# Kernel tuning notes

Measured on AMD Instinct MI355X. Metric: run time of the kernel, lower is better.

The kernel has to match this reference:

```python
import jax, jax.numpy as jnp
import numpy as np

N_NODES = 20000
N_EDGES = 200000
D_MODEL = 128
N_HEADS = 8
N_LAYERS = 2  # num_gnn - 1 concat layers


def setup_inputs() -> dict:
    key = jax.random.key(0)
    ks = jax.random.split(key, 12)
    s = 0.05  # keep activations well-scaled across residual layers
    hd = D_MODEL // N_HEADS  # 16
    return {
        "x": jax.random.normal(ks[0], (N_NODES, D_MODEL), jnp.float32),
        "src": jax.random.randint(ks[1], (N_EDGES,), 0, N_NODES),
        "dst": jax.random.randint(ks[2], (N_EDGES,), 0, N_NODES),
        "Ws": jax.random.normal(ks[3], (N_LAYERS, D_MODEL, D_MODEL), jnp.float32) * s,
        "als": jax.random.normal(ks[4], (N_LAYERS, N_HEADS, hd), jnp.float32) * s,
        "ars": jax.random.normal(ks[5], (N_LAYERS, N_HEADS, hd), jnp.float32) * s,
        "bs": jax.random.normal(ks[6], (N_LAYERS, D_MODEL), jnp.float32) * s,
        "W_last": jax.random.normal(ks[7], (D_MODEL, N_HEADS * D_MODEL), jnp.float32) * s,
        "al_last": jax.random.normal(ks[8], (N_HEADS, D_MODEL), jnp.float32) * s,
        "ar_last": jax.random.normal(ks[9], (N_HEADS, D_MODEL), jnp.float32) * s,
        "b_last": jax.random.normal(ks[10], (N_HEADS * D_MODEL,), jnp.float32) * s,
    }


def gat_conv(h, src, dst, W, al, ar, b, num_nodes):
    """DGL GATConv (eval mode, dropout off): returns (N, H, D) head outputs."""
    H, D = al.shape
    feat = (h @ W).reshape(num_nodes, H, D)          # (N,H,D)
    el = jnp.sum(feat * al[None], axis=-1)           # (N,H) attn on src side
    er = jnp.sum(feat * ar[None], axis=-1)           # (N,H) attn on dst side
    e = jax.nn.leaky_relu(el[src] + er[dst], 0.2)    # (E,H)
    # edge softmax over incoming edges of each dst node, per head
    m = jax.ops.segment_max(e, dst, num_segments=num_nodes)  # (N,H)
    p = jnp.exp(e - m[dst])                          # (E,H)
    z = jax.ops.segment_sum(p, dst, num_segments=num_nodes)  # (N,H)
    a = p / z[dst]                                   # (E,H)
    msg = feat[src] * a[..., None]                   # (E,H,D) weighted messages
    rst = jax.ops.segment_sum(msg, dst, num_segments=num_nodes)  # (N,H,D)
    return rst + b.reshape(1, H, D)


def reference(x, src, dst, Ws, als, ars, bs, W_last, al_last, ar_last, b_last):
    N = x.shape[0]
    h = x
    for i in range(N_LAYERS):
        temp = gat_conv(h, src, dst, Ws[i], als[i], ars[i], bs[i], N)  # (N,H,hd)
        h = h + jax.nn.elu(temp.reshape(N, -1))       # concat heads, ELU, residual
    temp = gat_conv(h, src, dst, W_last, al_last, ar_last, b_last, N)  # (N,H,D)
    h = h + jnp.mean(temp, axis=1)                    # mean over heads, residual
    return h
```

## Files before the change

### kernel.cpp

```cpp
#include <hip/hip_runtime.h>
#include <math.h>

#define N_NODES 20000
#define N_EDGES 200000
#define DM 128
#define NH 8

typedef __attribute__((ext_vector_type(8))) short bf16x8;
typedef __attribute__((ext_vector_type(4))) float f32x4;

__device__ __forceinline__ unsigned short f2b(float f) {
  unsigned int u = __float_as_uint(f);
  unsigned int r = (u + 0x7FFFu + ((u >> 16) & 1u)) >> 16;
  return (unsigned short)r;
}
__device__ __forceinline__ float b2f(unsigned short s) {
  return __uint_as_float(((unsigned int)s) << 16);
}

__global__ __launch_bounds__(256) void degzero(int* __restrict__ deg) {
  int i = blockIdx.x * 256 + threadIdx.x;
  if (i < N_NODES) deg[i] = 0;
}

__global__ __launch_bounds__(256) void prep_all(
    const float* __restrict__ x, float* __restrict__ h, unsigned short* __restrict__ hb,
    const int* __restrict__ dstE, int* __restrict__ deg, int* __restrict__ rank,
    const float* __restrict__ Ws, unsigned short* __restrict__ wsz,
    const float* __restrict__ W_last, unsigned short* __restrict__ wpsz,
    const float* __restrict__ al_last, const float* __restrict__ ar_last,
    const float* __restrict__ b_last, unsigned short* __restrict__ wlrsz,
    float* __restrict__ mb) {
  int i = blockIdx.x * 256 + threadIdx.x;
  if (i < (N_NODES * DM) / 4) {
    float4 v = ((const float4*)x)[i];
    ((float4*)h)[i] = v;
    ((ushort4*)hb)[i] = make_ushort4(f2b(v.x), f2b(v.y), f2b(v.z), f2b(v.w));
  }
  if (i < N_EDGES) rank[i] = atomicAdd(&deg[dstE[i]], 1);
  if (i < 2 * 16384) {
    int layer = i >> 14;
    int r = i & 16383;
    int j = r & 7, l = (r >> 3) & 63, f = (r >> 9) & 7, ks = r >> 12;
    int k = ks * 32 + ((l >> 4) << 3) + j;
    int n = f * 16 + (l & 15);
    wsz[i] = f2b(Ws[(size_t)layer * 16384 + k * 128 + n]);
  }
  if (i < 131072) {
    int j = i & 7, l = (i >> 3) & 63, f = (i >> 9) & 7, ks = i >> 12;
    int k = ks * 32 + ((l >> 4) << 3) + j;
    int n = f * 16 + (l & 15);
    int h_ = k >> 7, ko = k & 127;
    wpsz[i] = f2b(W_last[(size_t)ko * 1024 + h_ * 128 + n] * 0.125f);
  }
  if (i < 2048) {
    int j = i & 7, l = (i >> 3) & 63, ks = i >> 9;
    int k = ks * 32 + ((l >> 4) << 3) + j;
    int n = l & 15;
    int hh = n & 7;
    const float* av = (n < 8) ? (al_last + hh * 128) : (ar_last + hh * 128);
    float s = 0.f;
    for (int d = 0; d < 128; ++d) s += W_last[(size_t)k * 1024 + hh * 128 + d] * av[d];
    wlrsz[i] = f2b(s);
  }
  if (i < 128) {
    float s = 0.f;
#pragma unroll
    for (int hh = 0; hh < 8; ++hh) s += b_last[hh * 128 + i];
    mb[i] = s * 0.125f;
  }
}

template <int K>
__device__ __forceinline__ void dev_gemm(int tile, const unsigned short* __restrict__ A,
                                         const unsigned short* __restrict__ Bsz,
                                         unsigned short* __restrict__ Cb,
                                         const float* __restrict__ al,
                                         const float* __restrict__ ar,
                                         float* __restrict__ elr, int lane, int wid) {
  const int wrow = wid & 1, wc = wid >> 1;
  const int r0 = tile * 32;
  const int arow = r0 + wrow * 16 + (lane & 15);
  const int kg = lane >> 4;

  f32x4 acc[4];
#pragma unroll
  for (int fi = 0; fi < 4; ++fi) acc[fi] = {0.f, 0.f, 0.f, 0.f};

  const bf16x8* Ap = (const bf16x8*)(A + (size_t)arow * K + kg * 8);
#pragma unroll 4
  for (int ks = 0; ks < K / 32; ++ks) {
    bf16x8 a = Ap[ks * 4];
#pragma unroll
    for (int fi = 0; fi < 4; ++fi) {
      int f = wc * 4 + fi;
      bf16x8 b = *(const bf16x8*)(Bsz + (((size_t)(ks * 8 + f) * 64 + lane) << 3));
      acc[fi] = __builtin_amdgcn_mfma_f32_16x16x32_bf16(a, b, acc[fi], 0, 0, 0);
    }
  }

  const int rbase = r0 + wrow * 16 + (lane >> 4) * 4;
#pragma unroll
  for (int fi = 0; fi < 4; ++fi) {
    int col = wc * 64 + fi * 16 + (lane & 15);
#pragma unroll
    for (int r = 0; r < 4; ++r) {
      Cb[(size_t)(rbase + r) * DM + col] = f2b(acc[fi][r]);
    }
  }

#pragma unroll
  for (int fi = 0; fi < 4; ++fi) {
    int hh = wc * 4 + fi;
    float alv = al[hh * 16 + (lane & 15)];
    float arv = ar[hh * 16 + (lane & 15)];
#pragma unroll
    for (int r = 0; r < 4; ++r) {
      float pl = acc[fi][r] * alv;
      float pr = acc[fi][r] * arv;
#pragma unroll
      for (int msk = 1; msk < 16; msk <<= 1) {
        pl += __shfl_xor(pl, msk, 64);
        pr += __shfl_xor(pr, msk, 64);
      }
      if ((lane & 15) == 0) {
        int row = rbase + r;
        elr[row * 16 + hh] = pl;
        elr[row * 16 + 8 + hh] = pr;
      }
    }
  }
}

__global__ __launch_bounds__(256) void gemm0_scan(
    const unsigned short* __restrict__ A, const unsigned short* __restrict__ Bsz,
    unsigned short* __restrict__ Cb, const float* __restrict__ al,
    const float* __restrict__ ar, float* __restrict__ elr, const int* __restrict__ deg,
    int* __restrict__ off, int* __restrict__ bbase_g, int* __restrict__ bcur_g) {
  const int bid = blockIdx.x;
  const int GB = N_NODES / 32;
  if (bid < GB) {
    dev_gemm<DM>(bid, A, Bsz, Cb, al, ar, elr, threadIdx.x & 63, threadIdx.x >> 6);
    return;
  }
  __shared__ int part[256];
  __shared__ int hist[4][64];
  const int tid = threadIdx.x;
  const int wv = tid >> 6, lane = tid & 63;
  const int CHUNK = (N_NODES + 255) / 256;
  const int b0 = tid * CHUNK;
  const int b1 = min(N_NODES, b0 + CHUNK);
  if (tid < 64) {
    hist[0][tid] = 0; hist[1][tid] = 0; hist[2][tid] = 0; hist[3][tid] = 0;
  }
  __syncthreads();
  int s = 0;
  for (int idx = b0; idx < b1; ++idx) {
    int d = deg[idx];
    s += d;
    atomicAdd(&hist[wv][min(d, 63)], 1);
  }
  part[tid] = s;
  __syncthreads();
  for (int ofs = 1; ofs < 256; ofs <<= 1) {
    int v = (tid >= ofs) ? part[tid - ofs] : 0;
    __syncthreads();
    part[tid] += v;
    __syncthreads();
  }
  int run = (tid > 0) ? part[tid - 1] : 0;
  for (int idx = b0; idx < b1; ++idx) {
    off[idx] = run;
    run += deg[idx];
  }
  if (tid == 255) off[N_NODES] = part[255];
  if (wv == 0) {
    int c = hist[0][lane] + hist[1][lane] + hist[2][lane] + hist[3][lane];
    int inc = c;
#pragma unroll
    for (int ofs = 1; ofs < 64; ofs <<= 1) {
      int v = __shfl_up(inc, ofs, 64);
      if (lane >= ofs) inc += v;
    }
    bbase_g[lane] = inc - c;
    bcur_g[lane] = 0;
  }
}

__global__ __launch_bounds__(256) void scatter_both(
    const int* __restrict__ srcE, const int* __restrict__ dstE,
    const int* __restrict__ rank, const int* __restrict__ off, int* __restrict__ csr_src,
    const int* __restrict__ deg, const int* __restrict__ bbase_g,
    int* __restrict__ bcur_g, int* __restrict__ perm) {
  __shared__ int lcnt[64];
  __shared__ int gbase[64];
  const int bid = blockIdx.x;
  const int EB = (N_EDGES + 255) / 256;
  if (bid < EB) {
    int e = bid * 256 + threadIdx.x;
    if (e < N_EDGES) csr_src[off[dstE[e]] + rank[e]] = srcE[e];
  } else {
    const int tid = threadIdx.x;
    int idx = (bid - EB) * 256 + tid;
    if (tid < 64) lcnt[tid] = 0;
    __syncthreads();
    int d = 0, lrank = 0;
    bool valid = idx < N_NODES;
    if (valid) {
      d = min(deg[idx], 63);
      lrank = atomicAdd(&lcnt[d], 1);
    }
    __syncthreads();
    if (tid < 64 && lcnt[tid] > 0) gbase[tid] = atomicAdd(&bcur_g[tid], lcnt[tid]);
    __syncthreads();
    if (valid) perm[bbase_g[d] + gbase[d] + lrank] = idx;
  }
}

template <int MODE>
__global__ __launch_bounds__(256) void fused_small(
    const int* __restrict__ perm, const int* __restrict__ off,
    const int* __restrict__ csr_src, const unsigned short* __restrict__ feat,
    const float* __restrict__ elr, const float* __restrict__ bias, float* __restrict__ h,
    unsigned short* __restrict__ hb, const unsigned short* __restrict__ wsz1,
    const float* __restrict__ al1, const float* __restrict__ ar1,
    unsigned short* __restrict__ feat_out, float* __restrict__ elr_out,
    const unsigned short* __restrict__ wlrsz, float* __restrict__ elr2_out) {
  __shared__ float a_lds[4][64];
  __shared__ int s_lds[4][8];
  __shared__ float zi_lds[4][8];
  __shared__ __align__(16) unsigned short nh_lds[4][128];
  __shared__ int pnode[4];
  const int wid = threadIdx.x >> 6;
  const int t = perm[blockIdx.x * 4 + wid];
  const int lane = threadIdx.x & 63;
  const int e_loc = lane >> 3, hh = lane & 7;
  const int hg = lane >> 3;
  const int beg = off[t], end = off[t + 1];
  const float ert = elr[t * 16 + 8 + hh];
  if (lane == 0) pnode[wid] = t;

  int e = beg + e_loc;
  bool val = e < end;
  int s = val ? csr_src[e] : 0;
  float xl = val ? elr[s * 16 + hh] : 0.f;

  float z = 0.f, acc0 = 0.f, acc1 = 0.f;
  for (int base = beg; base < end; base += 8) {
    float ex = 0.f;
    if (val) {
      float xv = xl + ert;
      xv = xv > 0.f ? xv : 0.2f * xv;
      ex = __expf(xv);
    }
    a_lds[wid][lane] = ex;
    if (hh == 0) s_lds[wid][e_loc] = s;
    __builtin_amdgcn_wave_barrier();
    asm volatile("s_waitcnt lgkmcnt(0)" ::: "memory");
    z += ex;
    int en = base + 8 + e_loc;
    bool valn = en < end;
    int sn = valn ? csr_src[en] : 0;
    float xln = valn ? elr[sn * 16 + hh] : 0.f;
    int n = min(8, end - base);
    if (n == 8) {
#pragma unroll
      for (int e2 = 0; e2 < 8; ++e2) {
        int s2 = s_lds[wid][e2];
        float a = a_lds[wid][e2 * 8 + hg];
        unsigned int hv = *(const unsigned int*)&feat[(size_t)s2 * 128 + 2 * lane];
        acc0 += a * b2f((unsigned short)(hv & 0xffffu));
        acc1 += a * b2f((unsigned short)(hv >> 16));
      }
    } else {
      for (int e2 = 0; e2 < n; ++e2) {
        int s2 = s_lds[wid][e2];
        float a = a_lds[wid][e2 * 8 + hg];
        unsigned int hv = *(const unsigned int*)&feat[(size_t)s2 * 128 + 2 * lane];
        acc0 += a * b2f((unsigned short)(hv & 0xffffu));
        acc1 += a * b2f((unsigned short)(hv >> 16));
      }
    }
    __builtin_amdgcn_wave_barrier();
    s = sn;
    xl = xln;
    val = valn;
  }
  z += __shfl_xor(z, 8, 64);
  z += __shfl_xor(z, 16, 64);
  z += __shfl_xor(z, 32, 64);
  if (e_loc == 0) zi_lds[wid][hh] = (z > 0.f) ? 1.f / z : 0.f;
  __builtin_amdgcn_wave_barrier();
  asm volatile("s_waitcnt lgkmcnt(0)" ::: "memory");
  float zi = zi_lds[wid][hg];

  float2 bv = *(const float2*)&bias[2 * lane];
  float v0 = acc0 * zi + bv.x;
  float v1 = acc1 * zi + bv.y;
  v0 = v0 > 0.f ? v0 : expm1f(v0);
  v1 = v1 > 0.f ? v1 : expm1f(v1);
  size_t idx = (size_t)t * 128 + 2 * lane;
  float2 hv = *(const float2*)&h[idx];
  float nh0 = hv.x + v0;
  float nh1 = hv.y + v1;
  *(float2*)&h[idx] = make_float2(nh0, nh1);
  unsigned short b0 = f2b(nh0), b1 = f2b(nh1);
  *(ushort2*)&hb[idx] = make_ushort2(b0, b1);
  *(ushort2*)&nh_lds[wid][2 * lane] = make_ushort2(b0, b1);

  if (MODE == 1) {
    __builtin_amdgcn_wave_barrier();
    asm volatile("s_waitcnt lgkmcnt(0)" ::: "memory");
    const int kg = lane >> 4;
    f32x4 acc = {0.f, 0.f, 0.f, 0.f};
#pragma unroll
    for (int ks = 0; ks < 4; ++ks) {
      bf16x8 a = *(const bf16x8*)&nh_lds[wid][ks * 32 + kg * 8];
      bf16x8 b = *(const bf16x8*)(wlrsz + (((size_t)ks * 64 + lane) << 3));
      acc = __builtin_amdgcn_mfma_f32_16x16x32_bf16(a, b, acc, 0, 0, 0);
    }
    if (lane < 16) elr2_out[t * 16 + lane] = acc[0];
  }

  if (MODE == 0) {
    __syncthreads();
    const int r16 = lane & 15;
    const int kg = lane >> 4;
    f32x4 acc2[2];
    acc2[0] = {0.f, 0.f, 0.f, 0.f};
    acc2[1] = {0.f, 0.f, 0.f, 0.f};
#pragma unroll
    for (int ks = 0; ks < 4; ++ks) {
      bf16x8 a = {0, 0, 0, 0, 0, 0, 0, 0};
      if (r16 < 4) a = *(const bf16x8*)&nh_lds[r16][ks * 32 + kg * 8];
#pragma unroll
      for (int fi = 0; fi < 2; ++fi) {
        int f = wid * 2 + fi;
        bf16x8 b = *(const bf16x8*)(wsz1 + (((size_t)(ks * 8 + f) * 64 + lane) << 3));
        acc2[fi] = __builtin_amdgcn_mfma_f32_16x16x32_bf16(a, b, acc2[fi], 0, 0, 0);
      }
    }
    const int rowl = (lane >> 4) * 4;
#pragma unroll
    for (int fi = 0; fi < 2; ++fi) {
      int f = wid * 2 + fi;
      int col = f * 16 + r16;
      float alv = al1[col];
      float arv = ar1[col];
#pragma unroll
      for (int r = 0; r < 4; ++r) {
        float v = acc2[fi][r];
        if (rowl == 0) feat_out[(size_t)pnode[r] * 128 + col] = f2b(v);
        float pl = v * alv;
        float pr = v * arv;
#pragma unroll
        for (int msk = 1; msk < 16; msk <<= 1) {
          pl += __shfl_xor(pl, msk, 64);
          pr += __shfl_xor(pr, msk, 64);
        }
        if (r16 == 0 && rowl == 0) {
          int pn = pnode[r];
          elr_out[pn * 16 + f] = pl;
          elr_out[pn * 16 + 8 + f] = pr;
        }
      }
    }
  }
}

#define GT_STRIDE 1032
__global__ __launch_bounds__(1024) void agg_gemm16(
    const int* __restrict__ perm, const int* __restrict__ off,
    const int* __restrict__ csr_src, const unsigned short* __restrict__ hb,
    const float* __restrict__ elr, const unsigned short* __restrict__ wpsz,
    const float* __restrict__ hres, const float* __restrict__ mb,
    float* __restrict__ out) {
  __shared__ __align__(16) unsigned short gt[16][GT_STRIDE];
  __shared__ float red[8][64][4];
  __shared__ float a_lds[16][64];
  __shared__ float zi_lds[16][8];
  __shared__ int pnode[16];
  const int wid = threadIdx.x >> 6;
  const int lane = threadIdx.x & 63;
  const int t0 = blockIdx.x * 16;
  const int t = perm[t0 + wid];
  const int e_loc = lane >> 3, hh = lane & 7;
  if (lane == 0) pnode[wid] = t;

  {
    const int beg = off[t], end = off[t + 1];
    const float ert = elr[t * 16 + 8 + hh];

    int eA = beg + e_loc;
    bool vA = eA < end;
    int sA = vA ? csr_src[eA] : 0;
    float xA = vA ? elr[sA * 16 + hh] : 0.f;
    int eB = beg + 8 + e_loc;
    bool vB = eB < end;
    int sB = vB ? csr_src[eB] : 0;
    float xB = vB ? elr[sB * 16 + hh] : 0.f;

    unsigned int hvc[8];
    {
      int n0 = end - beg;
      if (n0 > 8) n0 = 8;
#pragma unroll
      for (int e2 = 0; e2 < 8; ++e2) {
        if (e2 < n0) {
          int s2 = __shfl(sA, e2 * 8, 64);
          hvc[e2] = *(const unsigned int*)&hb[(size_t)s2 * 128 + 2 * lane];
        }
      }
    }

    float z = 0.f;
    float accA[8], accB[8];
#pragma unroll
    for (int k = 0; k < 8; ++k) accA[k] = accB[k] = 0.f;

    for (int base = beg; base < end; base += 8) {
      float ex = 0.f;
      if (vA) {
        float xv = xA + ert;
        xv = xv > 0.f ? xv : 0.2f * xv;
        ex = __expf(xv);
      }
      a_lds[wid][lane] = ex;
      __builtin_amdgcn_wave_barrier();
      asm volatile("s_waitcnt lgkmcnt(0)" ::: "memory");
      z += ex;

      unsigned int hvn[8];
      int n1 = end - base - 8;
      if (n1 > 8) n1 = 8;
#pragma unroll
      for (int e2 = 0; e2 < 8; ++e2) {
        if (e2 < n1) {
          int s2 = __shfl(sB, e2 * 8, 64);
          hvn[e2] = *(const unsigned int*)&hb[(size_t)s2 * 128 + 2 * lane];
        }
      }
      int eC = base + 16 + e_loc;
      bool vC = eC < end;
      int sC = vC ? csr_src[eC] : 0;
      float xC = vC ? elr[sC * 16 + hh] : 0.f;

      int n = end - base;
      if (n > 8) n = 8;
#pragma unroll
      for (int e2 = 0; e2 < 8; ++e2) {
        if (e2 < n) {
          float4 pa = *(const float4*)&a_lds[wid][e2 * 8];
          float4 pb = *(const float4*)&a_lds[wid][e2 * 8 + 4];
          float h0 = b2f((unsigned short)(hvc[e2] & 0xffffu));
          float h1 = b2f((unsigned short)(hvc[e2] >> 16));
          accA[0] += pa.x * h0; accB[0] += pa.x * h1;
          accA[1] += pa.y * h0; accB[1] += pa.y * h1;
          accA[2] += pa.z * h0; accB[2] += pa.z * h1;
          accA[3] += pa.w * h0; accB[3] += pa.w * h1;
          accA[4] += pb.x * h0; accB[4] += pb.x * h1;
          accA[5] += pb.y * h0; accB[5] += pb.y * h1;
          accA[6] += pb.z * h0; accB[6] += pb.z * h1;
          accA[7] += pb.w * h0; accB[7] += pb.w * h1;
        }
      }
      __builtin_amdgcn_wave_barrier();
#pragma unroll
      for (int e2 = 0; e2 < 8; ++e2) hvc[e2] = hvn[e2];
      sA = sB; xA = xB; vA = vB;
      sB = sC; xB = xC; vB = vC;
    }
    z += __shfl_xor(z, 8, 64);
    z += __shfl_xor(z, 16, 64);
    z += __shfl_xor(z, 32, 64);
    if (e_loc == 0) zi_lds[wid][hh] = (z > 0.f) ? 1.f / z : 0.f;
    __builtin_amdgcn_wave_barrier();
    asm volatile("s_waitcnt lgkmcnt(0)" ::: "memory");
    float4 zia = *(const float4*)&zi_lds[wid][0];
    float4 zib = *(const float4*)&zi_lds[wid][4];
    float ziv[8] = {zia.x, zia.y, zia.z, zia.w, zib.x, zib.y, zib.z, zib.w};
#pragma unroll
    for (int h2 = 0; h2 < 8; ++h2) {
      *(ushort2*)&gt[wid][h2 * 128 + 2 * lane] =
          make_ushort2(f2b(accA[h2] * ziv[h2]), f2b(accB[h2] * ziv[h2]));
    }
  }
  __syncthreads();

  const int f = wid & 7;
  const int kh = wid >> 3;
  const int ar16 = lane & 15;
  const int kg = lane >> 4;
  f32x4 acc = {0.f, 0.f, 0.f, 0.f};
#pragma unroll 4
  for (int ksl = 0; ksl < 16; ++ksl) {
    int ks = kh * 16 + ksl;
    bf16x8 a = *(const bf16x8*)&gt[ar16][ks * 32 + kg * 8];
    bf16x8 b = *(const bf16x8*)(wpsz + (((size_t)(ks * 8 + f) * 64 + lane) << 3));
    acc = __builtin_amdgcn_mfma_f32_16x16x32_bf16(a, b, acc, 0, 0, 0);
  }
  if (kh == 1) {
    *(float4*)&red[f][lane][0] = make_float4(acc[0], acc[1], acc[2], acc[3]);
  }
  __syncthreads();
  if (kh == 0) {
    float4 p = *(const float4*)&red[f][lane][0];
    const int col = f * 16 + (lane & 15);
    const int rb = (lane >> 4) * 4;
    float r4[4] = {p.x, p.y, p.z, p.w};
#pragma unroll
    for (int r = 0; r < 4; ++r) {
      int row = pnode[rb + r];
      out[(size_t)row * 128 + col] =
          acc[r] + r4[r] + hres[(size_t)row * 128 + col] + mb[col];
    }
  }
}

extern "C" void kernel_launch(void* const* d_in, const int* in_sizes, int n_in,
                              void* d_out, int out_size, void* d_ws, size_t ws_size,
                              hipStream_t stream) {
  const float* x = (const float*)d_in[0];
  const int* src = (const int*)d_in[1];
  const int* dst = (const int*)d_in[2];
  const float* Ws = (const float*)d_in[3];
  const float* als = (const float*)d_in[4];
  const float* ars = (const float*)d_in[5];
  const float* bs = (const float*)d_in[6];
  const float* W_last = (const float*)d_in[7];
  const float* al_last = (const float*)d_in[8];
  const float* ar_last = (const float*)d_in[9];
  const float* b_last = (const float*)d_in[10];
  float* out = (float*)d_out;

  float* h = (float*)d_ws;
  float* elr0 = h + 2560000;
  float* elrB = elr0 + 320000;
  float* elr2 = elrB + 320000;
  float* mb = elr2 + 320000;
  unsigned short* hb = (unsigned short*)(mb + 128);
  unsigned short* featA = hb + 2560000;
  unsigned short* featB = featA + 2560000;
  unsigned short* wsz = featB + 2560000;
  unsigned short* wpsz = wsz + 32768;
  unsigned short* wlrsz = wpsz + 131072;
  int* deg = (int*)(wlrsz + 2048);
  int* off = deg + N_NODES;
  int* rank = off + N_NODES + 1;
  int* csr_src = rank + N_EDGES;
  int* perm = csr_src + N_EDGES;
  int* bbase_g = perm + N_NODES;
  int* bcur_g = bbase_g + 64;

  const int GB = N_NODES / 32;
  const int FB = N_NODES / 4;
  const int EB = (N_EDGES + 255) / 256;
  const int PB = (N_NODES + 255) / 256;

  degzero<<<(N_NODES + 255) / 256, 256, 0, stream>>>(deg);
  prep_all<<<(N_NODES * DM / 4 + 255) / 256, 256, 0, stream>>>(
      x, h, hb, dst, deg, rank, Ws, wsz, W_last, wpsz, al_last, ar_last, b_last, wlrsz, mb);
  gemm0_scan<<<GB + 1, 256, 0, stream>>>(hb, wsz, featA, als, ars, elr0, deg, off,
                                         bbase_g, bcur_g);
  scatter_both<<<EB + PB, 256, 0, stream>>>(src, dst, rank, off, csr_src, deg, bbase_g,
                                            bcur_g, perm);
  fused_small<0><<<FB, 256, 0, stream>>>(perm, off, csr_src, featA, elr0, bs, h, hb,
                                         wsz + 16384, als + 128, ars + 128, featB, elrB,
                                         nullptr, nullptr);
  fused_small<1><<<FB, 256, 0, stream>>>(perm, off, csr_src, featB, elrB, bs + 128, h, hb,
                                         nullptr, nullptr, nullptr, nullptr, nullptr,
                                         wlrsz, elr2);
  agg_gemm16<<<N_NODES / 16, 1024, 0, stream>>>(perm, off, csr_src, hb, elr2, wpsz, h, mb,
                                                out);
}
```

Measured before the change: 176.3 us.

## Split degree scan into standalone kernel and fuse GEMM with CSR scatter

The degree prefix scan moves out of the GEMM launch into its own single-block kernel of 1024 threads. The layer-0 GEMM is then merged with the edge scatter and node permutation into one launch, so the GEMM blocks overlap the scatter work. Previously the single scan block ran alongside the GEMM, and the scatter kernel had to wait for both. The launch count stays the same, but the serial scan now sits on the critical path before the GEMM, while the scatter no longer waits behind it.

```diff
diff --git a/kernel.cpp b/kernel.cpp
--- a/kernel.cpp
+++ b/kernel.cpp
@@ -71,6 +71,60 @@
   }
 }
 
+__global__ void scan_deg(const int* __restrict__ deg, int* __restrict__ off,
+                         int* __restrict__ bbase_g, int* __restrict__ bcur_g) {
+  __shared__ int part[1024];
+  __shared__ int hist[16][64];
+  const int tid = threadIdx.x;
+  const int wv = tid >> 6, lane = tid & 63;
+  const int CHUNK = (N_NODES + 1023) / 1024;
+  int base = tid * CHUNK;
+
+  for (int i = tid; i < 16 * 64; i += 1024) ((int*)hist)[i] = 0;
+  __syncthreads();
+
+  int s = 0;
+  for (int i = 0; i < CHUNK; ++i) {
+    int idx = base + i;
+    if (idx < N_NODES) {
+      int d = deg[idx];
+      s += d;
+      atomicAdd(&hist[wv][min(d, 63)], 1);
+    }
+  }
+  part[tid] = s;
+  __syncthreads();
+  for (int ofs = 1; ofs < 1024; ofs <<= 1) {
+    int v = (tid >= ofs) ? part[tid - ofs] : 0;
+    __syncthreads();
+    part[tid] += v;
+    __syncthreads();
+  }
+  int run = (tid > 0) ? part[tid - 1] : 0;
+  for (int i = 0; i < CHUNK; ++i) {
+    int idx = base + i;
+    if (idx < N_NODES) {
+      off[idx] = run;
+      run += deg[idx];
+    }
+  }
+  if (tid == 0) off[N_NODES] = part[1023];
+
+  if (wv == 0) {
+    int c = 0;
+#pragma unroll
+    for (int w = 0; w < 16; ++w) c += hist[w][lane];
+    int inc = c;
+#pragma unroll
+    for (int ofs = 1; ofs < 64; ofs <<= 1) {
+      int v = __shfl_up(inc, ofs, 64);
+      if (lane >= ofs) inc += v;
+    }
+    bbase_g[lane] = inc - c;
+    bcur_g[lane] = 0;
+  }
+}
+
 template <int K>
 __device__ __forceinline__ void dev_gemm(int tile, const unsigned short* __restrict__ A,
                                          const unsigned short* __restrict__ Bsz,
@@ -132,76 +186,28 @@
   }
 }
 
-__global__ __launch_bounds__(256) void gemm0_scan(
+__global__ __launch_bounds__(256) void gemm0_scatter(
     const unsigned short* __restrict__ A, const unsigned short* __restrict__ Bsz,
     unsigned short* __restrict__ Cb, const float* __restrict__ al,
-    const float* __restrict__ ar, float* __restrict__ elr, const int* __restrict__ deg,
-    int* __restrict__ off, int* __restrict__ bbase_g, int* __restrict__ bcur_g) {
-  const int bid = blockIdx.x;
-  const int GB = N_NODES / 32;
-  if (bid < GB) {
-    dev_gemm<DM>(bid, A, Bsz, Cb, al, ar, elr, threadIdx.x & 63, threadIdx.x >> 6);
-    return;
-  }
-  __shared__ int part[256];
-  __shared__ int hist[4][64];
-  const int tid = threadIdx.x;
-  const int wv = tid >> 6, lane = tid & 63;
-  const int CHUNK = (N_NODES + 255) / 256;
-  const int b0 = tid * CHUNK;
-  const int b1 = min(N_NODES, b0 + CHUNK);
-  if (tid < 64) {
-    hist[0][tid] = 0; hist[1][tid] = 0; hist[2][tid] = 0; hist[3][tid] = 0;
-  }
-  __syncthreads();
-  int s = 0;
-  for (int idx = b0; idx < b1; ++idx) {
-    int d = deg[idx];
-    s += d;
-    atomicAdd(&hist[wv][min(d, 63)], 1);
-  }
-  part[tid] = s;
-  __syncthreads();
-  for (int ofs = 1; ofs < 256; ofs <<= 1) {
-    int v = (tid >= ofs) ? part[tid - ofs] : 0;
-    __syncthreads();
-    part[tid] += v;
-    __syncthreads();
-  }
-  int run = (tid > 0) ? part[tid - 1] : 0;
-  for (int idx = b0; idx < b1; ++idx) {
-    off[idx] = run;
-    run += deg[idx];
-  }
-  if (tid == 255) off[N_NODES] = part[255];
-  if (wv == 0) {
-    int c = hist[0][lane] + hist[1][lane] + hist[2][lane] + hist[3][lane];
-    int inc = c;
-#pragma unroll
-    for (int ofs = 1; ofs < 64; ofs <<= 1) {
-      int v = __shfl_up(inc, ofs, 64);
-      if (lane >= ofs) inc += v;
-    }
-    bbase_g[lane] = inc - c;
-    bcur_g[lane] = 0;
-  }
-}
-
-__global__ __launch_bounds__(256) void scatter_both(
-    const int* __restrict__ srcE, const int* __restrict__ dstE,
-    const int* __restrict__ rank, const int* __restrict__ off, int* __restrict__ csr_src,
-    const int* __restrict__ deg, const int* __restrict__ bbase_g,
-    int* __restrict__ bcur_g, int* __restrict__ perm) {
+    const float* __restrict__ ar, float* __restrict__ elr, const int* __restrict__ srcE,
+    const int* __restrict__ dstE, const int* __restrict__ rank,
+    const int* __restrict__ off, int* __restrict__ csr_src, const int* __restrict__ deg,
+    const int* __restrict__ bbase_g, int* __restrict__ bcur_g, int* __restrict__ perm) {
   __shared__ int lcnt[64];
   __shared__ int gbase[64];
   const int bid = blockIdx.x;
+  const int GB = N_NODES / 32;
   const int EB = (N_EDGES + 255) / 256;
-  if (bid < EB) {
-    int e = bid * 256 + threadIdx.x;
-    if (e < N_EDGES) csr_src[off[dstE[e]] + rank[e]] = srcE[e];
+  if (bid < GB) {
+    dev_gemm<DM>(bid, A, Bsz, Cb, al, ar, elr, threadIdx.x & 63, threadIdx.x >> 6);
+  } else if (bid < GB + EB) {
+    int e = (bid - GB) * 256 + threadIdx.x;
+    if (e < N_EDGES) {
+      csr_src[off[dstE[e]] + rank[e]] = srcE[e];
+    }
   } else {
     const int tid = threadIdx.x;
-    int idx = (bid - EB) * 256 + tid;
+    int idx = (bid - GB - EB) * 256 + tid;
     if (tid < 64) lcnt[tid] = 0;
     __syncthreads();
     int d = 0, lrank = 0;
@@ -560,10 +566,10 @@
   degzero<<<(N_NODES + 255) / 256, 256, 0, stream>>>(deg);
   prep_all<<<(N_NODES * DM / 4 + 255) / 256, 256, 0, stream>>>(
       x, h, hb, dst, deg, rank, Ws, wsz, W_last, wpsz, al_last, ar_last, b_last, wlrsz, mb);
-  gemm0_scan<<<GB + 1, 256, 0, stream>>>(hb, wsz, featA, als, ars, elr0, deg, off,
-                                         bbase_g, bcur_g);
-  scatter_both<<<EB + PB, 256, 0, stream>>>(src, dst, rank, off, csr_src, deg, bbase_g,
-                                            bcur_g, perm);
+  scan_deg<<<1, 1024, 0, stream>>>(deg, off, bbase_g, bcur_g);
+  gemm0_scatter<<<GB + EB + PB, 256, 0, stream>>>(hb, wsz, featA, als, ars, elr0, src,
+                                                  dst, rank, off, csr_src, deg, bbase_g,
+                                                  bcur_g, perm);
   fused_small<0><<<FB, 256, 0, stream>>>(perm, off, csr_src, featA, elr0, bs, h, hb,
                                          wsz + 16384, als + 128, ars + 128, featB, elrB,
                                          nullptr, nullptr);
```

Result: faster. 164.5 us (median of 3 runs) (-6.7%).
